# Kernel tuning notes

Hardware: AMD Instinct MI355X
Metric: run time of the kernel (lower is better)

The kernel has to match this reference:

```python
import jax, jax.numpy as jnp
import numpy as np

NUM_HEADS = 16
INPUT_DIM = 1024  # == dim == qkv_scale


def setup_inputs() -> dict:
    key = jax.random.key(0)
    k1, k2, k3 = jax.random.split(key, 3)
    x = jax.random.normal(k1, (4, 2048, INPUT_DIM), dtype=jnp.float32)
    # torch Linear(input_dim, 3*dim): y = x @ W.T + b; we store W pre-transposed as [in, out]
    W_qkv = jax.random.normal(k2, (INPUT_DIM, 3 * INPUT_DIM), dtype=jnp.float32) * (INPUT_DIM ** -0.5)
    b_qkv = jax.random.normal(k3, (3 * INPUT_DIM,), dtype=jnp.float32) * 0.01
    return {"x": x, "W_qkv": W_qkv, "b_qkv": b_qkv}


def reference(x, W_qkv, b_qkv):
    b, n, _ = x.shape
    h = NUM_HEADS
    d = INPUT_DIM // h
    scale = INPUT_DIM ** 0.5  # qkv_scale**0.5, MULTIPLIED (no softmax, no division)

    qkv = x @ W_qkv + b_qkv                      # [b, n, 3*dim]
    # rearrange 'b n (h d k) -> k b h n d': last axis splits (h, d, 3), k fastest
    qkv = qkv.reshape(b, n, h, d, 3)
    q = jnp.transpose(qkv[..., 0], (0, 2, 1, 3))  # [b, h, n, d]
    k_ = jnp.transpose(qkv[..., 1], (0, 2, 1, 3))
    v = jnp.transpose(qkv[..., 2], (0, 2, 1, 3))

    attn = jnp.einsum('bhid,bhjd->bhij', q, k_) * scale  # [b, h, n, n]
    out = jnp.einsum('bhij,bhjd->bhid', attn, v)         # [b, h, n, d]
    return out
```

## Files before the change

### kernel.cpp

```cpp
#include <hip/hip_runtime.h>
#include <stdint.h>

#define DEV __device__ __forceinline__

typedef float f32x4 __attribute__((ext_vector_type(4)));
typedef __bf16 bf16x8 __attribute__((ext_vector_type(8)));
typedef short short8 __attribute__((ext_vector_type(8)));
typedef short short4v __attribute__((ext_vector_type(4)));

DEV unsigned short f2bf(float f) {
    union { float f; unsigned u; } c; c.f = f;
    unsigned u = c.u;
    u += 0x7fffu + ((u >> 16) & 1u);
    return (unsigned short)(u >> 16);
}
DEV void async_ld16(const void* g, void* l) {
    __builtin_amdgcn_global_load_lds(
        (const __attribute__((address_space(1))) unsigned int*)g,
        (__attribute__((address_space(3))) unsigned int*)l, 16, 0, 0);
}
DEV f32x4 mfma16(bf16x8 a, bf16x8 b, f32x4 c) {
    return __builtin_amdgcn_mfma_f32_16x16x32_bf16(a, b, c, 0, 0, 0);
}

__global__ __launch_bounds__(256) void k_prep(const float* __restrict__ x,
                                              const float* __restrict__ W,
                                              unsigned short* __restrict__ xb,
                                              unsigned short* __restrict__ Wt) {
    __shared__ float T[64][65];
    const int blk = blockIdx.x, t = threadIdx.x;
    if (blk < 4096) {
        int i = blk * 256 + t;
        const float4* xp = (const float4*)x;
        float4 a = xp[i * 2], b = xp[i * 2 + 1];
        short8 o;
        o[0] = (short)f2bf(a.x); o[1] = (short)f2bf(a.y);
        o[2] = (short)f2bf(a.z); o[3] = (short)f2bf(a.w);
        o[4] = (short)f2bf(b.x); o[5] = (short)f2bf(b.y);
        o[6] = (short)f2bf(b.z); o[7] = (short)f2bf(b.w);
        *(short8*)(xb + i * 8) = o;
    } else {
        int bx = blk - 4096;
        int k0 = (bx / 48) * 64, n0 = (bx % 48) * 64;
        int rr = t >> 4, c4 = (t & 15) * 4;
        for (int i = 0; i < 4; i++) {
            int row = rr + i * 16;
            float4 v = *(const float4*)(W + (unsigned)(k0 + row) * 3072u + n0 + c4);
            T[row][c4] = v.x; T[row][c4 + 1] = v.y; T[row][c4 + 2] = v.z; T[row][c4 + 3] = v.w;
        }
        __syncthreads();
        for (int i = 0; i < 4; i++) {
            int ncol = rr + i * 16;
            int n = n0 + ncol;
            int which = n % 3;
            int oc = (n / 192) * 64 + (n % 192) / 3;
            short4v o;
            o[0] = (short)f2bf(T[c4 + 0][ncol]);
            o[1] = (short)f2bf(T[c4 + 1][ncol]);
            o[2] = (short)f2bf(T[c4 + 2][ncol]);
            o[3] = (short)f2bf(T[c4 + 3][ncol]);
            *(short4v*)(Wt + (unsigned)which * 1048576u + (unsigned)oc * 1024u + k0 + c4) = o;
        }
    }
}

#define BARRIER() asm volatile("s_barrier" ::: "memory")
#define WAITV(n) do { asm volatile("s_waitcnt vmcnt(" #n ")" ::: "memory"); \
                      __builtin_amdgcn_sched_barrier(0); } while (0)

__global__ __launch_bounds__(256, 2) void k_qkv(const unsigned short* __restrict__ xb,
                                                const unsigned short* __restrict__ Wt,
                                                const float* __restrict__ bias,
                                                unsigned short* __restrict__ Qs,
                                                unsigned short* __restrict__ K,
                                                unsigned short* __restrict__ V) {
    __shared__ __align__(16) unsigned short As[2][128 * 64];
    __shared__ __align__(16) unsigned short Bs[2][128 * 64];

    const int o = blockIdx.x;
    const int w = (o & 7) * 192 + (o >> 3);
    const int mt = w / 24, nt = w % 24;
    const int m0 = mt * 128;
    const int plane = nt >> 3;
    const int pc0 = (nt & 7) * 128;
    const unsigned short* Xp = xb + (unsigned)m0 * 1024u;
    const unsigned short* Wp = Wt + (unsigned)plane * 1048576u + (unsigned)pc0 * 1024u;

    const int t = threadIdx.x;
    const int wave = t >> 6, lane = t & 63;
    const int lan15 = lane & 15, quad = lane >> 4;
    const int slr = wave * 32 + (lane >> 3);
    const int scs = lane & 7;

    const bool swp = (plane == 0);
    const int aw = (wave & 1) * 64;
    const int bw = (wave >> 1) * 64;

    f32x4 acc[4][4] = {};

#define STAGE(kt, b) do {                                                     \
        const int kk_ = (kt) * 64;                                            \
        _Pragma("unroll")                                                     \
        for (int i_ = 0; i_ < 4; i_++) {                                      \
            int r_ = slr + i_ * 8;                                            \
            int c_ = scs ^ (r_ & 7);                                          \
            async_ld16(Xp + (unsigned)r_ * 1024u + kk_ + c_ * 8,              \
                       (void*)(As[b] + (wave * 32 + i_ * 8) * 64));           \
            async_ld16(Wp + (unsigned)r_ * 1024u + kk_ + c_ * 8,              \
                       (void*)(Bs[b] + (wave * 32 + i_ * 8) * 64));           \
        }                                                                     \
    } while (0)

    STAGE(0, 0);

    for (int kt = 0; kt < 16; kt++) {
        const int buf = kt & 1;
        if (kt + 1 < 16) {
            STAGE(kt + 1, buf ^ 1);
            WAITV(8);
        } else {
            WAITV(0);
        }
        BARRIER();

        const unsigned short* Ab = (swp ? Bs[buf] : As[buf]) + aw * 64;
        const unsigned short* Bb = (swp ? As[buf] : Bs[buf]) + bw * 64;
#pragma unroll
        for (int ks = 0; ks < 2; ks++) {
            const int c0 = ks * 4 + quad;
            bf16x8 af[4], bfr[4];
#pragma unroll
            for (int tm = 0; tm < 4; tm++) {
                int row = tm * 16 + lan15;
                af[tm] = *(const bf16x8*)(Ab + row * 64 + (c0 ^ (row & 7)) * 8);
            }
#pragma unroll
            for (int tn = 0; tn < 4; tn++) {
                int row = tn * 16 + lan15;
                bfr[tn] = *(const bf16x8*)(Bb + row * 64 + (c0 ^ (row & 7)) * 8);
            }
#pragma unroll
            for (int tm = 0; tm < 4; tm++)
#pragma unroll
                for (int tn = 0; tn < 4; tn++)
                    acc[tm][tn] = mfma16(af[tm], bfr[tn], acc[tm][tn]);
        }
        BARRIER();
    }
#undef STAGE

    if (plane == 0) {
#pragma unroll
        for (int tm = 0; tm < 4; tm++) {
            int c4 = pc0 + aw + tm * 16 + quad * 4;
            int h = c4 >> 6, dd = c4 & 63;
            float b0 = bias[h * 192 + (dd + 0) * 3];
            float b1 = bias[h * 192 + (dd + 1) * 3];
            float b2 = bias[h * 192 + (dd + 2) * 3];
            float b3 = bias[h * 192 + (dd + 3) * 3];
#pragma unroll
            for (int tn = 0; tn < 4; tn++) {
                int token = m0 + bw + tn * 16 + lan15;
                unsigned bb = (unsigned)(token >> 11), tl = (unsigned)(token & 2047);
                uint2 p;
                p.x = (unsigned)f2bf((acc[tm][tn][0] + b0) * 32.0f) |
                      ((unsigned)f2bf((acc[tm][tn][1] + b1) * 32.0f) << 16);
                p.y = (unsigned)f2bf((acc[tm][tn][2] + b2) * 32.0f) |
                      ((unsigned)f2bf((acc[tm][tn][3] + b3) * 32.0f) << 16);
                *(uint2*)(Qs + bb * 2097152u + tl * 1024u + c4) = p;
            }
        }
    } else {
        unsigned short* dst = (plane == 1) ? K : V;
        const int batch = m0 >> 11;
#pragma unroll
        for (int tn = 0; tn < 4; tn++) {
            int cip = pc0 + bw + tn * 16 + lan15;
            int h = cip >> 6, d = cip & 63;
            float bv = bias[h * 192 + d * 3 + plane];
            unsigned kv_base = ((unsigned)(batch * 16 + h) * 64u + (unsigned)d) * 2048u;
#pragma unroll
            for (int tm = 0; tm < 4; tm++) {
                unsigned token0 = (unsigned)((m0 + aw + tm * 16 + quad * 4) & 2047);
                uint2 p;
                p.x = (unsigned)f2bf(acc[tm][tn][0] + bv) |
                      ((unsigned)f2bf(acc[tm][tn][1] + bv) << 16);
                p.y = (unsigned)f2bf(acc[tm][tn][2] + bv) |
                      ((unsigned)f2bf(acc[tm][tn][3] + bv) << 16);
                *(uint2*)(dst + kv_base + token0) = p;
            }
        }
    }
}

__global__ __launch_bounds__(256) void k_attn4(const unsigned short* __restrict__ Kt,
                                               const unsigned short* __restrict__ Vt,
                                               const unsigned short* __restrict__ Qs,
                                               float* __restrict__ out) {
    __shared__ __align__(16) unsigned short Ks[64 * 128];
    __shared__ __align__(16) unsigned short Vs[64 * 128];
    __shared__ __align__(16) unsigned short Msb[64 * 64];
    const int bh = blockIdx.x & 63, sub = blockIdx.x >> 6;
    const int b = bh >> 4, h = bh & 15;
    const int wave = threadIdx.x >> 6, lane = threadIdx.x & 63;
    const int lan15 = lane & 15, quad = lane >> 4;
    const unsigned base = (unsigned)bh * 131072u;
    const int mt0 = (wave & 1) * 2, nt0 = (wave >> 1) * 2;
    const int slr = wave * 16 + (lane >> 4), scs = lane & 15;

    f32x4 macc[2][2] = {};
    for (int j = 0; j < 16; j++) {
        __syncthreads();
        for (int i = 0; i < 4; i++) {
            int lr = slr + i * 4;
            int c = scs ^ (lr & 15);
            async_ld16(Kt + base + (unsigned)lr * 2048u + j * 128 + c * 8,
                       (void*)(Ks + (wave * 16 + i * 4) * 128));
            async_ld16(Vt + base + (unsigned)lr * 2048u + j * 128 + c * 8,
                       (void*)(Vs + (wave * 16 + i * 4) * 128));
        }
        __syncthreads();
        for (int ks2 = 0; ks2 < 4; ks2++) {
            int c0 = ks2 * 4 + quad;
            bf16x8 ak[2], bv[2];
            for (int i = 0; i < 2; i++) {
                int row = (mt0 + i) * 16 + lan15;
                ak[i] = *(const bf16x8*)(Ks + row * 128 + (c0 ^ (row & 15)) * 8);
            }
            for (int i = 0; i < 2; i++) {
                int row = (nt0 + i) * 16 + lan15;
                bv[i] = *(const bf16x8*)(Vs + row * 128 + (c0 ^ (row & 15)) * 8);
            }
            for (int i = 0; i < 2; i++)
                for (int j2 = 0; j2 < 2; j2++)
                    macc[i][j2] = mfma16(ak[i], bv[j2], macc[i][j2]);
        }
    }
    for (int i = 0; i < 2; i++)
        for (int j2 = 0; j2 < 2; j2++) {
            int d2 = (nt0 + j2) * 16 + lan15;
            int c4 = ((mt0 + i) * 4 + quad) ^ (d2 & 15);
            uint2 p;
            p.x = (unsigned)f2bf(macc[i][j2][0]) | ((unsigned)f2bf(macc[i][j2][1]) << 16);
            p.y = (unsigned)f2bf(macc[i][j2][2]) | ((unsigned)f2bf(macc[i][j2][3]) << 16);
            *(uint2*)(Msb + d2 * 64 + c4 * 4) = p;
        }
    __syncthreads();

    const int t0 = sub * 256 + wave * 64;
    f32x4 oacc[4][4] = {};
#pragma unroll
    for (int ks = 0; ks < 2; ks++) {
        bf16x8 af[4], bfr[4];
        for (int mt = 0; mt < 4; mt++) {
            int tok = t0 + mt * 16 + lan15;
            af[mt] = *(const bf16x8*)(Qs + (unsigned)b * 2097152u + (unsigned)tok * 1024u +
                                      h * 64 + ks * 32 + quad * 8);
        }
        for (int nt = 0; nt < 4; nt++) {
            int d2 = nt * 16 + lan15;
            int cA = ks * 8 + quad * 2;
            uint2 u0 = *(const uint2*)(Msb + d2 * 64 + ((cA) ^ (d2 & 15)) * 4);
            uint2 u1 = *(const uint2*)(Msb + d2 * 64 + ((cA + 1) ^ (d2 & 15)) * 4);
            union { uint4 u; bf16x8 v; } cv;
            cv.u.x = u0.x; cv.u.y = u0.y; cv.u.z = u1.x; cv.u.w = u1.y;
            bfr[nt] = cv.v;
        }
        for (int mt = 0; mt < 4; mt++)
            for (int nt = 0; nt < 4; nt++)
                oacc[mt][nt] = mfma16(af[mt], bfr[nt], oacc[mt][nt]);
    }
    for (int mt = 0; mt < 4; mt++)
        for (int nt = 0; nt < 4; nt++)
            for (int r = 0; r < 4; r++)
                out[base + (unsigned)(t0 + mt * 16 + quad * 4 + r) * 64u + nt * 16 + lan15] =
                    oacc[mt][nt][r];
}

extern "C" void kernel_launch(void* const* d_in, const int* in_sizes, int n_in,
                              void* d_out, int out_size, void* d_ws, size_t ws_size,
                              hipStream_t stream) {
    const float* x = (const float*)d_in[0];
    const float* W = (const float*)d_in[1];
    const float* b = (const float*)d_in[2];
    float* out = (float*)d_out;

    unsigned short* xb = (unsigned short*)d_ws;
    unsigned short* Wt = xb + 8388608;
    unsigned short* Qs = Wt + 3145728;
    unsigned short* Kt = Qs + 8388608;
    unsigned short* Vt = Kt + 8388608;

    k_prep<<<4864, 256, 0, stream>>>(x, W, xb, Wt);
    k_qkv<<<1536, 256, 0, stream>>>(xb, Wt, b, Qs, Kt, Vt);
    k_attn4<<<512, 256, 0, stream>>>(Kt, Vt, Qs, out);
}
```

Measured before the change: 182.0 us.

## Enlarge QKV GEMM tile to 256x256 with 512-thread blocks

The QKV projection GEMM moves from 128x128 tiles with 256 threads to 256x256 tiles with 512 threads (8 waves, each computing 128x64). It launches 384 blocks instead of 1536 and remaps the block-to-tile swizzle. The larger tile raises arithmetic intensity and cuts redundant global/LDS loads, and MFMA sections are wrapped in s_setprio to favor matrix issue. The cost is 64KB LDS per block and 128 accumulator floats per thread, which adds register pressure and may reduce occupancy, and 384 blocks may fill the GPU's CUs less evenly.

```diff
diff --git a/kernel.cpp b/kernel.cpp
--- a/kernel.cpp
+++ b/kernel.cpp
@@ -68,46 +68,46 @@
 #define WAITV(n) do { asm volatile("s_waitcnt vmcnt(" #n ")" ::: "memory"); \
                       __builtin_amdgcn_sched_barrier(0); } while (0)
 
-__global__ __launch_bounds__(256, 2) void k_qkv(const unsigned short* __restrict__ xb,
+__global__ __launch_bounds__(512, 2) void k_qkv(const unsigned short* __restrict__ xb,
                                                 const unsigned short* __restrict__ Wt,
                                                 const float* __restrict__ bias,
                                                 unsigned short* __restrict__ Qs,
                                                 unsigned short* __restrict__ K,
                                                 unsigned short* __restrict__ V) {
-    __shared__ __align__(16) unsigned short As[2][128 * 64];
-    __shared__ __align__(16) unsigned short Bs[2][128 * 64];
+    __shared__ __align__(16) unsigned short As[2][256 * 64];
+    __shared__ __align__(16) unsigned short Bs[2][256 * 64];
 
     const int o = blockIdx.x;
-    const int w = (o & 7) * 192 + (o >> 3);
-    const int mt = w / 24, nt = w % 24;
-    const int m0 = mt * 128;
-    const int plane = nt >> 3;
-    const int pc0 = (nt & 7) * 128;
+    const int w = (o & 7) * 48 + (o >> 3);
+    const int mtile = w & 31, ntile = w >> 5;
+    const int m0 = mtile * 256;
+    const int plane = ntile >> 2;
+    const int pc0 = (ntile & 3) * 256;
     const unsigned short* Xp = xb + (unsigned)m0 * 1024u;
     const unsigned short* Wp = Wt + (unsigned)plane * 1048576u + (unsigned)pc0 * 1024u;
 
     const int t = threadIdx.x;
     const int wave = t >> 6, lane = t & 63;
     const int lan15 = lane & 15, quad = lane >> 4;
-    const int slr = wave * 32 + (lane >> 3);
-    const int scs = lane & 7;
+    const int slr = t >> 3;
+    const int scs = t & 7;
 
     const bool swp = (plane == 0);
-    const int aw = (wave & 1) * 64;
-    const int bw = (wave >> 1) * 64;
-
-    f32x4 acc[4][4] = {};
-
-#define STAGE(kt, b) do {                                                     \
-        const int kk_ = (kt) * 64;                                            \
+    const int aRow0 = (wave & 1) * 128;
+    const int bRow0 = (wave >> 1) * 64;
+
+    f32x4 acc[8][4] = {};
+
+#define STAGE(kt, bf) do {                                                    \
+        const unsigned ko_ = (unsigned)((kt) * 64);                           \
         _Pragma("unroll")                                                     \
         for (int i_ = 0; i_ < 4; i_++) {                                      \
-            int r_ = slr + i_ * 8;                                            \
+            int r_ = i_ * 64 + slr;                                           \
             int c_ = scs ^ (r_ & 7);                                          \
-            async_ld16(Xp + (unsigned)r_ * 1024u + kk_ + c_ * 8,              \
-                       (void*)(As[b] + (wave * 32 + i_ * 8) * 64));           \
-            async_ld16(Wp + (unsigned)r_ * 1024u + kk_ + c_ * 8,              \
-                       (void*)(Bs[b] + (wave * 32 + i_ * 8) * 64));           \
+            async_ld16(Xp + (unsigned)r_ * 1024u + ko_ + c_ * 8,              \
+                       (void*)(As[bf] + (i_ * 64 + wave * 8) * 64));          \
+            async_ld16(Wp + (unsigned)r_ * 1024u + ko_ + c_ * 8,              \
+                       (void*)(Bs[bf] + (i_ * 64 + wave * 8) * 64));          \
         }                                                                     \
     } while (0)
 
@@ -115,44 +115,44 @@
 
     for (int kt = 0; kt < 16; kt++) {
         const int buf = kt & 1;
-        if (kt + 1 < 16) {
-            STAGE(kt + 1, buf ^ 1);
-            WAITV(8);
-        } else {
-            WAITV(0);
-        }
+        if (kt < 15) { STAGE(kt + 1, buf ^ 1); WAITV(8); }
+        else         { WAITV(0); }
         BARRIER();
 
-        const unsigned short* Ab = (swp ? Bs[buf] : As[buf]) + aw * 64;
-        const unsigned short* Bb = (swp ? As[buf] : Bs[buf]) + bw * 64;
+        const unsigned short* Aop = swp ? Bs[buf] : As[buf];
+        const unsigned short* Bop = swp ? As[buf] : Bs[buf];
 #pragma unroll
         for (int ks = 0; ks < 2; ks++) {
             const int c0 = ks * 4 + quad;
-            bf16x8 af[4], bfr[4];
-#pragma unroll
-            for (int tm = 0; tm < 4; tm++) {
-                int row = tm * 16 + lan15;
-                af[tm] = *(const bf16x8*)(Ab + row * 64 + (c0 ^ (row & 7)) * 8);
-            }
+            bf16x8 af[8], bfr[4];
 #pragma unroll
             for (int tn = 0; tn < 4; tn++) {
-                int row = tn * 16 + lan15;
-                bfr[tn] = *(const bf16x8*)(Bb + row * 64 + (c0 ^ (row & 7)) * 8);
-            }
-#pragma unroll
-            for (int tm = 0; tm < 4; tm++)
+                int row = bRow0 + tn * 16 + lan15;
+                bfr[tn] = *(const bf16x8*)(Bop + row * 64 + (c0 ^ (row & 7)) * 8);
+            }
+#pragma unroll
+            for (int tm = 0; tm < 8; tm++) {
+                int row = aRow0 + tm * 16 + lan15;
+                af[tm] = *(const bf16x8*)(Aop + row * 64 + (c0 ^ (row & 7)) * 8);
+            }
+            __builtin_amdgcn_s_setprio(1);
+#pragma unroll
+            for (int tm = 0; tm < 8; tm++)
 #pragma unroll
                 for (int tn = 0; tn < 4; tn++)
                     acc[tm][tn] = mfma16(af[tm], bfr[tn], acc[tm][tn]);
+            __builtin_amdgcn_s_setprio(0);
         }
         BARRIER();
     }
 #undef STAGE
 
     if (plane == 0) {
-#pragma unroll
-        for (int tm = 0; tm < 4; tm++) {
-            int c4 = pc0 + aw + tm * 16 + quad * 4;
+        const int cg = (wave & 1) * 128;
+        const int tg = (wave >> 1) * 64;
+#pragma unroll
+        for (int tm = 0; tm < 8; tm++) {
+            int c4 = pc0 + cg + tm * 16 + quad * 4;
             int h = c4 >> 6, dd = c4 & 63;
             float b0 = bias[h * 192 + (dd + 0) * 3];
             float b1 = bias[h * 192 + (dd + 1) * 3];
@@ -160,7 +160,7 @@
             float b3 = bias[h * 192 + (dd + 3) * 3];
 #pragma unroll
             for (int tn = 0; tn < 4; tn++) {
-                int token = m0 + bw + tn * 16 + lan15;
+                int token = m0 + tg + tn * 16 + lan15;
                 unsigned bb = (unsigned)(token >> 11), tl = (unsigned)(token & 2047);
                 uint2 p;
                 p.x = (unsigned)f2bf((acc[tm][tn][0] + b0) * 32.0f) |
@@ -172,16 +172,18 @@
         }
     } else {
         unsigned short* dst = (plane == 1) ? K : V;
+        const int tg = (wave & 1) * 128;
+        const int cg = (wave >> 1) * 64;
         const int batch = m0 >> 11;
 #pragma unroll
         for (int tn = 0; tn < 4; tn++) {
-            int cip = pc0 + bw + tn * 16 + lan15;
+            int cip = pc0 + cg + tn * 16 + lan15;
             int h = cip >> 6, d = cip & 63;
             float bv = bias[h * 192 + d * 3 + plane];
             unsigned kv_base = ((unsigned)(batch * 16 + h) * 64u + (unsigned)d) * 2048u;
 #pragma unroll
-            for (int tm = 0; tm < 4; tm++) {
-                unsigned token0 = (unsigned)((m0 + aw + tm * 16 + quad * 4) & 2047);
+            for (int tm = 0; tm < 8; tm++) {
+                unsigned token0 = (unsigned)((m0 + tg + tm * 16 + quad * 4) & 2047);
                 uint2 p;
                 p.x = (unsigned)f2bf(acc[tm][tn][0] + bv) |
                       ((unsigned)f2bf(acc[tm][tn][1] + bv) << 16);
@@ -292,6 +294,6 @@
     unsigned short* Vt = Kt + 8388608;
 
     k_prep<<<4864, 256, 0, stream>>>(x, W, xb, Wt);
-    k_qkv<<<1536, 256, 0, stream>>>(xb, Wt, b, Qs, Kt, Vt);
+    k_qkv<<<384, 512, 0, stream>>>(xb, Wt, b, Qs, Kt, Vt);
     k_attn4<<<512, 256, 0, stream>>>(Kt, Vt, Qs, out);
 }
```

Result: slower. 191.9 us (+5.5%).
